# Kernel optimization log

Hardware: AMD Instinct MI355X
Metric: run time of the kernel (lower is better)

Reference implementation:

```python
import jax, jax.numpy as jnp
import numpy as np

H = 32        # query heads
HKV = 8       # kv heads
D = 64        # head_dim
EPS = 1e-6    # rms_norm_eps
LAYER_IDX = 8
LAMBDA_INIT = float(0.8 - 0.6 * np.exp(-0.3 * LAYER_IDX))
NEG = -1e9


def rotate_half(x):
    x1, x2 = jnp.split(x, 2, axis=-1)
    return jnp.concatenate([-x2, x1], axis=-1)


def setup_inputs() -> dict:
    key = jax.random.key(0)
    ks = jax.random.split(key, 10)
    B, S, HID = 1, 2048, 2048
    hidden_states = jax.random.normal(ks[0], (B, S, HID), jnp.float32)
    # rotary embeddings (HF llama style): cos/sin [S, D]
    inv_freq = 1.0 / (10000.0 ** (np.arange(0, D, 2, dtype=np.float64) / D))
    freqs = np.outer(np.arange(S, dtype=np.float64), inv_freq)
    emb = np.concatenate([freqs, freqs], axis=-1)
    cos = jnp.asarray(np.cos(emb), jnp.float32)
    sin = jnp.asarray(np.sin(emb), jnp.float32)
    w = 0.02
    Wq = w * jax.random.normal(ks[1], (H * D, HID), jnp.float32)
    Wk = w * jax.random.normal(ks[2], (HKV * D, HID), jnp.float32)
    Wv = w * jax.random.normal(ks[3], (HKV * D, HID), jnp.float32)
    Wo = w * jax.random.normal(ks[4], (HID, H * D), jnp.float32)
    lam_std = 0.1
    lambda_q1 = lam_std * jax.random.normal(ks[5], (D,), jnp.float32)
    lambda_k1 = lam_std * jax.random.normal(ks[6], (D,), jnp.float32)
    lambda_q2 = lam_std * jax.random.normal(ks[7], (D,), jnp.float32)
    lambda_k2 = lam_std * jax.random.normal(ks[8], (D,), jnp.float32)
    return dict(hidden_states=hidden_states, cos=cos, sin=sin, Wq=Wq, Wk=Wk,
                Wv=Wv, Wo=Wo, lambda_q1=lambda_q1, lambda_k1=lambda_k1,
                lambda_q2=lambda_q2, lambda_k2=lambda_k2)


def reference(hidden_states, cos, sin, Wq, Wk, Wv, Wo,
              lambda_q1, lambda_k1, lambda_q2, lambda_k2):
    B, S, _ = hidden_states.shape
    # projections -> [B, H, S, D]
    q = (hidden_states @ Wq.T).reshape(B, S, H, D).transpose(0, 2, 1, 3)
    k = (hidden_states @ Wk.T).reshape(B, S, HKV, D).transpose(0, 2, 1, 3)
    v = (hidden_states @ Wv.T).reshape(B, S, HKV, D).transpose(0, 2, 1, 3)
    # RoPE (cos/sin broadcast over batch/head dims)
    q = q * cos + rotate_half(q) * sin
    k = k * cos + rotate_half(k) * sin
    # GQA repeat_kv: each kv head repeated consecutively
    g = H // HKV
    k = jnp.repeat(k, g, axis=1)
    v = jnp.repeat(v, g, axis=1)
    # differential value: concat first/second half of heads along feature dim
    v_cat = jnp.concatenate([v[:, :H // 2], v[:, H // 2:]], axis=-1)  # [B,H/2,S,2D]
    v_rep = jnp.tile(v_cat, (1, 2, 1, 1))                              # [B,H,S,2D]
    # causal attention (flash-attn is_causal, dropout=0 at eval)
    scores = jnp.einsum('bhqd,bhkd->bhqk', q, k) / np.sqrt(D)
    causal = jnp.tril(jnp.ones((S, S), bool))
    scores = jnp.where(causal, scores, NEG)
    probs = jax.nn.softmax(scores.astype(jnp.float32), axis=-1).astype(q.dtype)
    out = jnp.einsum('bhqk,bhkd->bhqd', probs, v_rep)  # [B,H,S,2D]
    out1, out2 = out[:, :H // 2], out[:, H // 2:]
    lam1 = jnp.exp(jnp.sum(lambda_q1 * lambda_k1))
    lam2 = jnp.exp(jnp.sum(lambda_q2 * lambda_k2))
    lam = lam1 - lam2 + LAMBDA_INIT
    a = out1 - lam * out2                               # [B,H/2,S,2D]
    # RMSNorm over 2D, no affine
    a = a * jax.lax.rsqrt(jnp.mean(a * a, axis=-1, keepdims=True) + EPS)
    a = (1.0 - LAMBDA_INIT) * a
    a = a.transpose(0, 2, 1, 3).reshape(B, S, H * D)
    return a @ Wo.T
```

## Files before the change

### kernel.cpp

```cpp
#include <hip/hip_runtime.h>

typedef unsigned short u16;
typedef __attribute__((ext_vector_type(8))) short v8s;
typedef __attribute__((ext_vector_type(4))) float v4f;

#define S_LEN 2048
#define HID   2048
#define NH    32
#define NKV   8
#define HD    64
#define DVV   128
#define LAMBDA_INIT  0.7455692280263525f
#define ONE_MINUS_LI 0.2544307719736475f

__device__ __forceinline__ u16 f2b(float f){
  union { float f; unsigned int i; } v; v.f = f;
  unsigned int x = v.i;
  unsigned int r = (x + 0x7fffu + ((x >> 16) & 1u)) >> 16;
  return (u16)r;
}
__device__ __forceinline__ float b2f(u16 u){
  union { unsigned int i; float f; } v; v.i = ((unsigned int)u) << 16; return v.f;
}

__device__ __forceinline__ void gld16(const u16* g, u16* l){
  __builtin_amdgcn_global_load_lds(
      (const __attribute__((address_space(1))) unsigned int*)g,
      (__attribute__((address_space(3))) unsigned int*)l, 16, 0, 0);
}

__global__ __launch_bounds__(256) void cast5(
    const float* __restrict__ hs, const float* __restrict__ Wq,
    const float* __restrict__ Wk, const float* __restrict__ Wv,
    const float* __restrict__ Wo,
    u16* __restrict__ hsb, u16* __restrict__ Wqkvb, u16* __restrict__ Wob)
{
  int b = blockIdx.x;
  const float* S; u16* D; int rb;
  if (b < 2048)      { S = hs; D = hsb;             rb = b; }
  else if (b < 4096) { S = Wq; D = Wqkvb;           rb = b - 2048; }
  else if (b < 4608) { S = Wk; D = Wqkvb + 4194304; rb = b - 4096; }
  else if (b < 5120) { S = Wv; D = Wqkvb + 5242880; rb = b - 4608; }
  else               { S = Wo; D = Wob;             rb = b - 5120; }
  size_t i = ((size_t)rb * 256 + threadIdx.x) * 8;
  float4 a = *(const float4*)(S + i);
  float4 c = *(const float4*)(S + i + 4);
  u16 o[8] = {f2b(a.x), f2b(a.y), f2b(a.z), f2b(a.w), f2b(c.x), f2b(c.y), f2b(c.z), f2b(c.w)};
  *(uint4*)(D + i) = *(const uint4*)o;
}

template<int MODE>
__global__ __launch_bounds__(256) void gemm_bf16(const u16* __restrict__ A, const u16* __restrict__ B,
                                                 void* __restrict__ Cv, int M, int N, int K,
                                                 const float* __restrict__ cosb, const float* __restrict__ sinb,
                                                 u16* __restrict__ Qbf, u16* __restrict__ Kbf)
{
  __shared__ __attribute__((aligned(16))) u16 As[2][128*64];
  __shared__ __attribute__((aligned(16))) u16 Bs[2][64*64];
  const int t    = threadIdx.x;
  const int w    = t >> 6, lane = t & 63;
  const int mm   = lane & 15, g = lane >> 4;
  const int m0   = blockIdx.y * 128, n0 = blockIdx.x * 64;
  const int lr   = lane >> 3;
  const int sch  = lane & 7;

  v4f acc[2][4];
#pragma unroll
  for (int i = 0; i < 2; i++)
#pragma unroll
    for (int j = 0; j < 4; j++) acc[i][j] = (v4f){0.f,0.f,0.f,0.f};

#define G_STAGE(kk, buf) do { \
    _Pragma("unroll") \
    for (int i = 0; i < 4; i++){ \
      int r  = w*32 + lr + i*8; \
      int ce = ((sch ^ (r & 7)) * 8); \
      gld16(A + (size_t)(m0 + r) * K + (kk) + ce, &As[buf][w*2048 + i*512]); \
    } \
    _Pragma("unroll") \
    for (int i = 0; i < 2; i++){ \
      int r  = w*16 + lr + i*8; \
      int ce = ((sch ^ (r & 7)) * 8); \
      gld16(B + (size_t)(n0 + r) * K + (kk) + ce, &Bs[buf][w*1024 + i*512]); \
    } \
  } while(0)

  G_STAGE(0, 0);
  __syncthreads();

  for (int k0 = 0; k0 < K; k0 += 64){
    const int cur = (k0 >> 6) & 1;
    if (k0){
      asm volatile("s_waitcnt vmcnt(0)" ::: "memory");
      __builtin_amdgcn_s_barrier();
      __builtin_amdgcn_sched_barrier(0);
    }
    if (k0 + 64 < K) G_STAGE(k0 + 64, cur ^ 1);

#pragma unroll
    for (int kc = 0; kc < 2; kc++){
      v8s af[2], bf[4];
#pragma unroll
      for (int i = 0; i < 2; i++){
        int r = w*32 + i*16 + mm;
        af[i] = *(const v8s*)&As[cur][r*64 + (((kc*4 + g) ^ (r & 7)) * 8)];
      }
#pragma unroll
      for (int j = 0; j < 4; j++){
        int r = j*16 + mm;
        bf[j] = *(const v8s*)&Bs[cur][r*64 + (((kc*4 + g) ^ (r & 7)) * 8)];
      }
#pragma unroll
      for (int i = 0; i < 2; i++)
#pragma unroll
        for (int j = 0; j < 4; j++)
          acc[i][j] = __builtin_amdgcn_mfma_f32_16x16x32_bf16(af[i], bf[j], acc[i][j], 0, 0, 0);
    }
  }
#undef G_STAGE

  if (MODE == 2 && n0 < 2560){
    u16* base = (n0 < 2048) ? (Qbf + (size_t)(n0 >> 6) * S_LEN * HD)
                            : (Kbf + (size_t)((n0 - 2048) >> 6) * S_LEN * HD);
#pragma unroll
    for (int i = 0; i < 2; i++)
#pragma unroll
      for (int j = 0; j < 2; j++)
#pragma unroll
        for (int r = 0; r < 4; r++){
          int s = m0 + w*32 + i*16 + g*4 + r;
          int d = j*16 + mm;
          float x1 = acc[i][j][r], x2 = acc[i][j+2][r];
          float c1 = cosb[s*HD + d],      s1 = sinb[s*HD + d];
          float c2 = cosb[s*HD + d + 32], s2 = sinb[s*HD + d + 32];
          base[(size_t)s*HD + d]      = f2b(x1*c1 - x2*s1);
          base[(size_t)s*HD + d + 32] = f2b(x2*c2 + x1*s2);
        }
  } else if (MODE != 0){
    u16* C = (u16*)Cv;
#pragma unroll
    for (int i = 0; i < 2; i++)
#pragma unroll
      for (int j = 0; j < 4; j++)
#pragma unroll
        for (int r = 0; r < 4; r++)
          C[(size_t)(m0 + w*32 + i*16 + g*4 + r) * N + n0 + j*16 + mm] = f2b(acc[i][j][r]);
  } else {
    float* C = (float*)Cv;
#pragma unroll
    for (int i = 0; i < 2; i++)
#pragma unroll
      for (int j = 0; j < 4; j++)
#pragma unroll
        for (int r = 0; r < 4; r++)
          C[(size_t)(m0 + w*32 + i*16 + g*4 + r) * N + n0 + j*16 + mm] = acc[i][j][r];
  }
}

__global__ __launch_bounds__(256) void vtrans(const u16* __restrict__ Vb, int stride, u16* __restrict__ Vt)
{
  __shared__ u16 T[64][72];
  const int b = blockIdx.x;
  const int h = b >> 5;
  const int s0 = (b & 31) * 64;
  const int t = threadIdx.x;
#pragma unroll
  for (int i = 0; i < 4; i++){
    int u = t + i * 256;
    int r = u >> 4, c4 = (u & 15) * 4;
    uint2 v = *(const uint2*)&Vb[(size_t)(s0 + r) * stride + h * HD + c4];
    T[c4+0][r] = (u16)(v.x & 0xffff); T[c4+1][r] = (u16)(v.x >> 16);
    T[c4+2][r] = (u16)(v.y & 0xffff); T[c4+3][r] = (u16)(v.y >> 16);
  }
  __syncthreads();
#pragma unroll
  for (int i = 0; i < 2; i++){
    int u = t + i * 256;
    int d = u >> 3, ch = (u & 7) * 8;
    *(uint4*)&Vt[((size_t)h * HD + d) * S_LEN + s0 + ch] = *(const uint4*)&T[d][ch];
  }
}

__global__ __launch_bounds__(512) void attn_fused(
    const u16* __restrict__ Qbf, const u16* __restrict__ Kbf, const u16* __restrict__ Vt,
    const float* __restrict__ lq1, const float* __restrict__ lk1,
    const float* __restrict__ lq2, const float* __restrict__ lk2,
    u16* __restrict__ Ctx)
{
  __shared__ __attribute__((aligned(16))) u16 SM[41984];
  u16* QPa = SM;
  u16* QPb = SM + 4608;
  u16* Ksf = SM + 9216;
  u16* Vs  = SM + 25600;
  float* OLDS = (float*)(SM + 9216);

  const int p   = blockIdx.x;
  const int hp  = blockIdx.y;
  const int kva = hp >> 2, kvb = kva + 4;
  const int t   = threadIdx.x, w = t >> 6, lane = t & 63;
  const int hb  = w >> 2;
  const int wq  = w & 3;
  const int mm  = lane & 15, g = lane >> 4, g8 = g * 8;
  const int sr  = t >> 3;
  const int sc  = t & 7;
  const int so  = sc * 8;
  const int x0  = ((g ^ (mm & 7)) * 8);
  const int x1  = (((g + 4) ^ (mm & 7)) * 8);

  u16* QP = hb ? QPb : QPa;

  float lp1 = lq1[lane] * lk1[lane];
  float lp2 = lq2[lane] * lk2[lane];
#pragma unroll
  for (int off = 1; off < 64; off <<= 1){
    lp1 += __shfl_xor(lp1, off);
    lp2 += __shfl_xor(lp2, off);
  }
  const float lam = __expf(lp1) - __expf(lp2) + LAMBDA_INIT;

  for (int seg = 0; seg < 2; seg++){
    const int qt = seg ? p : (31 - p);
    const int q0 = qt * 64;

    __syncthreads();
    {
      int ce = ((sc ^ (sr & 7)) * 8);
      gld16(Kbf + ((size_t)kva * S_LEN + sr) * HD + ce, Ksf + (w*8)*64);
      gld16(Kbf + ((size_t)kvb * S_LEN + sr) * HD + ce, Ksf + 8192 + (w*8)*64);
      gld16(Vt + ((size_t)kva * HD + sr) * S_LEN + ce, Vs + (w*8)*64);
      gld16(Vt + ((size_t)kvb * HD + sr) * S_LEN + ce, Vs + (w*8 + 64)*64);
    }
    *(uint4*)&QPa[sr*72 + so] = *(const uint4*)&Qbf[((size_t)hp        * S_LEN + q0 + sr) * HD + so];
    *(uint4*)&QPb[sr*72 + so] = *(const uint4*)&Qbf[((size_t)(hp + 16) * S_LEN + q0 + sr) * HD + so];
    __syncthreads();
    v8s qa0 = *(const v8s*)&QP[(wq*16 + mm)*72 + g8];
    v8s qa1 = *(const v8s*)&QP[(wq*16 + mm)*72 + 32 + g8];

    v4f O[8];
#pragma unroll
    for (int n = 0; n < 8; n++) O[n] = (v4f){0.f,0.f,0.f,0.f};
    float l[4] = {0.f,0.f,0.f,0.f};

    for (int k0 = 0; k0 <= q0; k0 += 64){
      const int cur = (k0 >> 6) & 1;
      if (k0){
        asm volatile("s_waitcnt vmcnt(0)" ::: "memory");
        __builtin_amdgcn_s_barrier();
        __builtin_amdgcn_sched_barrier(0);
      }
      if (k0 + 64 <= q0){
        int ce = ((sc ^ (sr & 7)) * 8);
        gld16(Vt + ((size_t)kva * HD + sr) * S_LEN + k0 + 64 + ce, Vs + (cur^1)*8192 + (w*8)*64);
        gld16(Vt + ((size_t)kvb * HD + sr) * S_LEN + k0 + 64 + ce, Vs + (cur^1)*8192 + (w*8 + 64)*64);
        gld16(Kbf + ((size_t)kva * S_LEN + k0 + 64 + sr) * HD + ce, Ksf + (cur^1)*4096 + (w*8)*64);
        gld16(Kbf + ((size_t)kvb * S_LEN + k0 + 64 + sr) * HD + ce, Ksf + 8192 + (cur^1)*4096 + (w*8)*64);
      }

      const u16* Kh = Ksf + hb*8192 + cur*4096;
      const bool dg = (k0 == q0);
      v4f S[4];
      __builtin_amdgcn_s_setprio(1);
#pragma unroll
      for (int n = 0; n < 4; n++){
        int row = n*16 + mm;
        v8s kb0 = *(const v8s*)&Kh[row*64 + x0];
        v8s kb1 = *(const v8s*)&Kh[row*64 + x1];
        v4f z = (v4f){0.f,0.f,0.f,0.f};
        z = __builtin_amdgcn_mfma_f32_16x16x32_bf16(qa0, kb0, z, 0, 0, 0);
        z = __builtin_amdgcn_mfma_f32_16x16x32_bf16(qa1, kb1, z, 0, 0, 0);
        S[n] = z;
      }
      __builtin_amdgcn_s_setprio(0);
#pragma unroll
      for (int n = 0; n < 4; n++)
#pragma unroll
        for (int r = 0; r < 4; r++){
          float pe = __expf(S[n][r] * 0.125f);
          if (dg && (n*16 + mm > wq*16 + g*4 + r)) pe = 0.f;
          l[r] += pe;
          QP[(wq*16 + g*4 + r)*72 + n*16 + mm] = f2b(pe);
        }
      v8s pa0 = *(const v8s*)&QP[(wq*16 + mm)*72 + g8];
      v8s pa1 = *(const v8s*)&QP[(wq*16 + mm)*72 + 32 + g8];
      const u16* Vh = Vs + cur*8192;
      __builtin_amdgcn_s_setprio(1);
#pragma unroll
      for (int n = 0; n < 8; n++){
        int row = n*16 + mm;
        v8s vb0 = *(const v8s*)&Vh[row*64 + x0];
        v8s vb1 = *(const v8s*)&Vh[row*64 + x1];
        O[n] = __builtin_amdgcn_mfma_f32_16x16x32_bf16(pa0, vb0, O[n], 0, 0, 0);
        O[n] = __builtin_amdgcn_mfma_f32_16x16x32_bf16(pa1, vb1, O[n], 0, 0, 0);
      }
      __builtin_amdgcn_s_setprio(0);
    }

#pragma unroll
    for (int off = 1; off < 16; off <<= 1)
#pragma unroll
      for (int r = 0; r < 4; r++)
        l[r] += __shfl_xor(l[r], off);
    float il[4];
#pragma unroll
    for (int r = 0; r < 4; r++) il[r] = hb ? (lam / l[r]) : (1.0f / l[r]);

    __syncthreads();
    if (hb){
#pragma unroll
      for (int n = 0; n < 8; n++)
#pragma unroll
        for (int r = 0; r < 4; r++)
          OLDS[(wq*16 + g*4 + r)*128 + n*16 + mm] = O[n][r] * il[r];
    }
    __syncthreads();
    if (!hb){
      float av[8][4];
      float ss[4] = {0.f,0.f,0.f,0.f};
#pragma unroll
      for (int n = 0; n < 8; n++)
#pragma unroll
        for (int r = 0; r < 4; r++){
          float a = O[n][r] * il[r] - OLDS[(wq*16 + g*4 + r)*128 + n*16 + mm];
          av[n][r] = a;
          ss[r] += a * a;
        }
#pragma unroll
      for (int off = 1; off < 16; off <<= 1)
#pragma unroll
        for (int r = 0; r < 4; r++)
          ss[r] += __shfl_xor(ss[r], off);
      float rv[4];
#pragma unroll
      for (int r = 0; r < 4; r++)
        rv[r] = rsqrtf(ss[r] * (1.0f/128.0f) + 1e-6f) * ONE_MINUS_LI;
#pragma unroll
      for (int n = 0; n < 8; n++)
#pragma unroll
        for (int r = 0; r < 4; r++){
          int srow = q0 + wq*16 + g*4 + r;
          Ctx[(size_t)srow * HID + hp * DVV + n*16 + mm] = f2b(av[n][r] * rv[r]);
        }
    }
  }
}

extern "C" void kernel_launch(void* const* d_in, const int* in_sizes, int n_in,
                              void* d_out, int out_size, void* d_ws, size_t ws_size,
                              hipStream_t stream)
{
  (void)in_sizes; (void)n_in; (void)out_size; (void)ws_size;
  const float* hs   = (const float*)d_in[0];
  const float* cosb = (const float*)d_in[1];
  const float* sinb = (const float*)d_in[2];
  const float* Wq   = (const float*)d_in[3];
  const float* Wk   = (const float*)d_in[4];
  const float* Wv   = (const float*)d_in[5];
  const float* Wo   = (const float*)d_in[6];
  const float* lq1  = (const float*)d_in[7];
  const float* lk1  = (const float*)d_in[8];
  const float* lq2  = (const float*)d_in[9];
  const float* lk2  = (const float*)d_in[10];

  char* ws = (char*)d_ws;
  u16* hsb   = (u16*)(ws);
  u16* Wqkvb = (u16*)(ws + (8u  << 20));
  u16* QKVb  = (u16*)(ws + (20u << 20));
  u16* Ctx   = (u16*)(ws + (20u << 20));
  u16* Wob   = (u16*)(ws + (32u << 20));
  u16* Kbf   = (u16*)(ws + (44u << 20));
  u16* Vt    = (u16*)(ws + (46u << 20));
  u16* Qbf   = (u16*)(ws + (48u << 20));

  cast5<<<7168, 256, 0, stream>>>(hs, Wq, Wk, Wv, Wo, hsb, Wqkvb, Wob);
  gemm_bf16<2><<<dim3(48, 16), 256, 0, stream>>>(hsb, Wqkvb, QKVb, S_LEN, 3072, HID,
                                                 cosb, sinb, Qbf, Kbf);
  vtrans<<<NKV * (S_LEN/64), 256, 0, stream>>>(QKVb + 2560, 3072, Vt);
  attn_fused<<<dim3(16, 16), 512, 0, stream>>>(Qbf, Kbf, Vt, lq1, lk1, lq2, lk2, Ctx);
  gemm_bf16<0><<<dim3(32, 16), 256, 0, stream>>>(Ctx, Wob, (float*)d_out, S_LEN, 2048, HID,
                                                 nullptr, nullptr, nullptr, nullptr);
}
```

Before: 225.1 us.

## Fuse V transpose into QKV GEMM epilogue and triple-buffer attention K/V loads

The QKV GEMM epilogue for the V columns now transposes the tile through shared memory and writes V directly in [head, d, seq] layout. This removes the separate vtrans kernel and its launch plus an extra round trip of V through global memory. The attention kernel moves from double to 4-slot K/V buffering with a prefetch distance of two tiles, waiting on vmcnt(4) instead of draining all loads. In exchange the attention kernel's LDS use grows to about 146 KB, which may limit occupancy.

Result: no change. 221.0 us (-1.8%).

```diff
diff --git a/kernel.cpp b/kernel.cpp
--- a/kernel.cpp
+++ b/kernel.cpp
@@ -53,7 +53,8 @@
 __global__ __launch_bounds__(256) void gemm_bf16(const u16* __restrict__ A, const u16* __restrict__ B,
                                                  void* __restrict__ Cv, int M, int N, int K,
                                                  const float* __restrict__ cosb, const float* __restrict__ sinb,
-                                                 u16* __restrict__ Qbf, u16* __restrict__ Kbf)
+                                                 u16* __restrict__ Qbf, u16* __restrict__ Kbf,
+                                                 u16* __restrict__ Vtp)
 {
   __shared__ __attribute__((aligned(16))) u16 As[2][128*64];
   __shared__ __attribute__((aligned(16))) u16 Bs[2][64*64];
@@ -136,15 +137,27 @@
           base[(size_t)s*HD + d]      = f2b(x1*c1 - x2*s1);
           base[(size_t)s*HD + d + 32] = f2b(x2*c2 + x1*s2);
         }
-  } else if (MODE != 0){
-    u16* C = (u16*)Cv;
+  } else if (MODE == 2){
+    __syncthreads();
+    u16* T = (u16*)As;
+    const int h = (n0 - 2560) >> 6;
 #pragma unroll
     for (int i = 0; i < 2; i++)
 #pragma unroll
       for (int j = 0; j < 4; j++)
 #pragma unroll
-        for (int r = 0; r < 4; r++)
-          C[(size_t)(m0 + w*32 + i*16 + g*4 + r) * N + n0 + j*16 + mm] = f2b(acc[i][j][r]);
+        for (int r = 0; r < 4; r++){
+          int s = w*32 + i*16 + g*4 + r;
+          int d = j*16 + mm;
+          T[d*136 + s] = f2b(acc[i][j][r]);
+        }
+    __syncthreads();
+#pragma unroll
+    for (int it = 0; it < 4; it++){
+      int u  = t + it*256;
+      int d  = u >> 4, ch = (u & 15) * 8;
+      *(uint4*)&Vtp[((size_t)h*HD + d)*S_LEN + m0 + ch] = *(const uint4*)&T[d*136 + ch];
+    }
   } else {
     float* C = (float*)Cv;
 #pragma unroll
@@ -154,30 +167,6 @@
 #pragma unroll
         for (int r = 0; r < 4; r++)
           C[(size_t)(m0 + w*32 + i*16 + g*4 + r) * N + n0 + j*16 + mm] = acc[i][j][r];
-  }
-}
-
-__global__ __launch_bounds__(256) void vtrans(const u16* __restrict__ Vb, int stride, u16* __restrict__ Vt)
-{
-  __shared__ u16 T[64][72];
-  const int b = blockIdx.x;
-  const int h = b >> 5;
-  const int s0 = (b & 31) * 64;
-  const int t = threadIdx.x;
-#pragma unroll
-  for (int i = 0; i < 4; i++){
-    int u = t + i * 256;
-    int r = u >> 4, c4 = (u & 15) * 4;
-    uint2 v = *(const uint2*)&Vb[(size_t)(s0 + r) * stride + h * HD + c4];
-    T[c4+0][r] = (u16)(v.x & 0xffff); T[c4+1][r] = (u16)(v.x >> 16);
-    T[c4+2][r] = (u16)(v.y & 0xffff); T[c4+3][r] = (u16)(v.y >> 16);
-  }
-  __syncthreads();
-#pragma unroll
-  for (int i = 0; i < 2; i++){
-    int u = t + i * 256;
-    int d = u >> 3, ch = (u & 7) * 8;
-    *(uint4*)&Vt[((size_t)h * HD + d) * S_LEN + s0 + ch] = *(const uint4*)&T[d][ch];
   }
 }
 
@@ -187,11 +176,11 @@
     const float* __restrict__ lq2, const float* __restrict__ lk2,
     u16* __restrict__ Ctx)
 {
-  __shared__ __attribute__((aligned(16))) u16 SM[41984];
+  __shared__ __attribute__((aligned(16))) u16 SM[74752];
   u16* QPa = SM;
   u16* QPb = SM + 4608;
   u16* Ksf = SM + 9216;
-  u16* Vs  = SM + 25600;
+  u16* Vs  = SM + 41984;
   float* OLDS = (float*)(SM + 9216);
 
   const int p   = blockIdx.x;
@@ -206,6 +195,7 @@
   const int so  = sc * 8;
   const int x0  = ((g ^ (mm & 7)) * 8);
   const int x1  = (((g + 4) ^ (mm & 7)) * 8);
+  const int ce  = ((sc ^ (sr & 7)) * 8);
 
   u16* QP = hb ? QPb : QPa;
 
@@ -218,18 +208,21 @@
   }
   const float lam = __expf(lp1) - __expf(lp2) + LAMBDA_INIT;
 
+#define TILE_ISSUE(kk) do { \
+    const int tb_ = ((kk) >> 6) & 3; \
+    gld16(Kbf + ((size_t)kva * S_LEN + (kk) + sr) * HD + ce, Ksf + tb_*4096 + (w*8)*64); \
+    gld16(Kbf + ((size_t)kvb * S_LEN + (kk) + sr) * HD + ce, Ksf + 16384 + tb_*4096 + (w*8)*64); \
+    gld16(Vt  + ((size_t)kva * HD + sr) * S_LEN + (kk) + ce, Vs + tb_*8192 + (w*8)*64); \
+    gld16(Vt  + ((size_t)kvb * HD + sr) * S_LEN + (kk) + ce, Vs + tb_*8192 + (w*8 + 64)*64); \
+  } while(0)
+
   for (int seg = 0; seg < 2; seg++){
     const int qt = seg ? p : (31 - p);
     const int q0 = qt * 64;
 
     __syncthreads();
-    {
-      int ce = ((sc ^ (sr & 7)) * 8);
-      gld16(Kbf + ((size_t)kva * S_LEN + sr) * HD + ce, Ksf + (w*8)*64);
-      gld16(Kbf + ((size_t)kvb * S_LEN + sr) * HD + ce, Ksf + 8192 + (w*8)*64);
-      gld16(Vt + ((size_t)kva * HD + sr) * S_LEN + ce, Vs + (w*8)*64);
-      gld16(Vt + ((size_t)kvb * HD + sr) * S_LEN + ce, Vs + (w*8 + 64)*64);
-    }
+    TILE_ISSUE(0);
+    if (64 <= q0) TILE_ISSUE(64);
     *(uint4*)&QPa[sr*72 + so] = *(const uint4*)&Qbf[((size_t)hp        * S_LEN + q0 + sr) * HD + so];
     *(uint4*)&QPb[sr*72 + so] = *(const uint4*)&Qbf[((size_t)(hp + 16) * S_LEN + q0 + sr) * HD + so];
     __syncthreads();
@@ -242,21 +235,16 @@
     float l[4] = {0.f,0.f,0.f,0.f};
 
     for (int k0 = 0; k0 <= q0; k0 += 64){
-      const int cur = (k0 >> 6) & 1;
+      const int cur = (k0 >> 6) & 3;
       if (k0){
-        asm volatile("s_waitcnt vmcnt(0)" ::: "memory");
+        if (k0 + 64 <= q0) asm volatile("s_waitcnt vmcnt(4)" ::: "memory");
+        else               asm volatile("s_waitcnt vmcnt(0)" ::: "memory");
         __builtin_amdgcn_s_barrier();
         __builtin_amdgcn_sched_barrier(0);
       }
-      if (k0 + 64 <= q0){
-        int ce = ((sc ^ (sr & 7)) * 8);
-        gld16(Vt + ((size_t)kva * HD + sr) * S_LEN + k0 + 64 + ce, Vs + (cur^1)*8192 + (w*8)*64);
-        gld16(Vt + ((size_t)kvb * HD + sr) * S_LEN + k0 + 64 + ce, Vs + (cur^1)*8192 + (w*8 + 64)*64);
-        gld16(Kbf + ((size_t)kva * S_LEN + k0 + 64 + sr) * HD + ce, Ksf + (cur^1)*4096 + (w*8)*64);
-        gld16(Kbf + ((size_t)kvb * S_LEN + k0 + 64 + sr) * HD + ce, Ksf + 8192 + (cur^1)*4096 + (w*8)*64);
-      }
-
-      const u16* Kh = Ksf + hb*8192 + cur*4096;
+      if (k0 + 128 <= q0) TILE_ISSUE(k0 + 128);
+
+      const u16* Kh = Ksf + hb*16384 + cur*4096;
       const bool dg = (k0 == q0);
       v4f S[4];
       __builtin_amdgcn_s_setprio(1);
@@ -294,6 +282,7 @@
       }
       __builtin_amdgcn_s_setprio(0);
     }
+#undef TILE_ISSUE
 
 #pragma unroll
     for (int off = 1; off < 16; off <<= 1)
@@ -364,7 +353,6 @@
   char* ws = (char*)d_ws;
   u16* hsb   = (u16*)(ws);
   u16* Wqkvb = (u16*)(ws + (8u  << 20));
-  u16* QKVb  = (u16*)(ws + (20u << 20));
   u16* Ctx   = (u16*)(ws + (20u << 20));
   u16* Wob   = (u16*)(ws + (32u << 20));
   u16* Kbf   = (u16*)(ws + (44u << 20));
@@ -372,10 +360,9 @@
   u16* Qbf   = (u16*)(ws + (48u << 20));
 
   cast5<<<7168, 256, 0, stream>>>(hs, Wq, Wk, Wv, Wo, hsb, Wqkvb, Wob);
-  gemm_bf16<2><<<dim3(48, 16), 256, 0, stream>>>(hsb, Wqkvb, QKVb, S_LEN, 3072, HID,
-                                                 cosb, sinb, Qbf, Kbf);
-  vtrans<<<NKV * (S_LEN/64), 256, 0, stream>>>(QKVb + 2560, 3072, Vt);
+  gemm_bf16<2><<<dim3(48, 16), 256, 0, stream>>>(hsb, Wqkvb, nullptr, S_LEN, 3072, HID,
+                                                 cosb, sinb, Qbf, Kbf, Vt);
   attn_fused<<<dim3(16, 16), 512, 0, stream>>>(Qbf, Kbf, Vt, lq1, lk1, lq2, lk2, Ctx);
   gemm_bf16<0><<<dim3(32, 16), 256, 0, stream>>>(Ctx, Wob, (float*)d_out, S_LEN, 2048, HID,
-                                                 nullptr, nullptr, nullptr, nullptr);
-}
+                                                 nullptr, nullptr, nullptr, nullptr, nullptr);
+}
```
